# Kernel tuning notes

Measured on AMD Instinct MI355X. Metric: run time of the kernel, lower is better.

The kernel has to match this reference:

```python
import jax, jax.numpy as jnp
import numpy as np

N = 20000      # nodes
E = 320000     # edges
F = 128        # feat_dim
N_RBF = 20
CUTOFF = 5.0


def setup_inputs() -> dict:
    key = jax.random.key(0)
    ks = jax.random.split(key, 12)
    h_i = jax.random.normal(ks[0], (N, F), dtype=jnp.float32)
    v_i = jax.random.normal(ks[1], (N, F, 3), dtype=jnp.float32)
    # distances in (0, cutoff); keep strictly > 0 to avoid div-by-zero in sinc basis
    d_ij = (jax.random.uniform(ks[2], (E,), dtype=jnp.float32) * 0.98 + 0.01) * CUTOFF
    r = jax.random.normal(ks[3], (E, 3), dtype=jnp.float32)
    unit_r_ij = r / jnp.linalg.norm(r, axis=-1, keepdims=True)
    nbrs = jax.random.randint(ks[4], (E, 2), 0, N, dtype=jnp.int64)
    # params: layers = Dense(F->F, swish) then Dense(F->3F); dist_embed dense: n_rbf -> 3F
    s1 = 1.0 / np.sqrt(F)
    W1 = jax.random.uniform(ks[5], (F, F), jnp.float32, -s1, s1)
    b1 = jax.random.uniform(ks[6], (F,), jnp.float32, -s1, s1)
    W2 = jax.random.uniform(ks[7], (F, 3 * F), jnp.float32, -s1, s1)
    b2 = jax.random.uniform(ks[8], (3 * F,), jnp.float32, -s1, s1)
    sr = 1.0 / np.sqrt(N_RBF)
    Wr = jax.random.uniform(ks[9], (N_RBF, 3 * F), jnp.float32, -sr, sr)
    br = jax.random.uniform(ks[10], (3 * F,), jnp.float32, -sr, sr)
    return {"h_i": h_i, "v_i": v_i, "d_ij": d_ij, "unit_r_ij": unit_r_ij,
            "nbrs": nbrs, "W1": W1, "b1": b1, "W2": W2, "b2": b2, "Wr": Wr, "br": br}


def _dist_embed(d, Wr, br):
    # PaiNN sinc-like radial basis: sin(n*pi*d/cutoff)/d, n=1..N_RBF
    n = jnp.arange(1, N_RBF + 1, dtype=d.dtype)
    rbf = jnp.sin(n[None, :] * jnp.pi * d[:, None] / CUTOFF) / d[:, None]  # [E, N_RBF]
    # cosine cutoff envelope
    fcut = 0.5 * (jnp.cos(jnp.pi * d / CUTOFF) + 1.0) * (d < CUTOFF)       # [E]
    return (rbf @ Wr + br) * fcut[:, None]                                  # [E, 3F]


def reference(h_i, v_i, d_ij, unit_r_ij, nbrs, W1, b1, W2, b2, Wr, br):
    # phi = Dense(swish) -> Dense : [N, 3F]
    phi = jax.nn.silu(h_i @ W1 + b1) @ W2 + b2
    src = nbrs[:, 1]
    dst = nbrs[:, 0]
    edge_inv = phi[src] * _dist_embed(d_ij, Wr, br)          # [E, 3F]
    edge_inv = edge_inv.reshape(edge_inv.shape[0], 3, F)     # [E, 3, F]
    f1, f2, f3 = edge_inv[:, 0], edge_inv[:, 1], edge_inv[:, 2]
    # dv: [E, F, 3]
    dv = f1[:, :, None] * unit_r_ij[:, None, :] + f2[:, :, None] * v_i[src]
    dh_i = jax.ops.segment_sum(f3, dst, num_segments=N)      # [N, F]
    dv_i = jax.ops.segment_sum(dv, dst, num_segments=N)      # [N, F, 3]
    return (dh_i, dv_i)
```

## Files before the change

kernel.cpp:

```cpp
#include <hip/hip_runtime.h>
#include <math.h>

#define F 128
#define THREEF 384
#define N_RBF 20
#define CUTOFF 5.0f
#define CAP 64
#define TLDS_STRIDE 136

typedef __bf16 bf16x8 __attribute__((ext_vector_type(8)));
typedef float  f32x4  __attribute__((ext_vector_type(4)));

__global__ __launch_bounds__(256) void prep_kernel(
    const float* __restrict__ d_ij, const float* __restrict__ unit_r,
    const int* __restrict__ nbrs,
    const float* __restrict__ W1, const float* __restrict__ W2,
    const float* __restrict__ Wr,
    int* __restrict__ cnt, float* __restrict__ pack,
    __bf16* __restrict__ W1T, __bf16* __restrict__ W2T,
    float* __restrict__ WrT, int E, int EB)
{
    const int tid = threadIdx.x;
    const int b   = blockIdx.x;

    if (b < EB) {
        const int e = b * 256 + tid;
        if (e >= E) return;
        const int2 nb = ((const int2*)nbrs)[e];
        const int dst = nb.x;
        const int src = nb.y;
        const int slot = atomicAdd(&cnt[dst], 1);
        if (slot >= CAP) return;

        const float d = d_ij[e];
        const float x = (float)M_PI * d * (1.0f / CUTOFF);
        float sx, cx;
        __sincosf(x, &sx, &cx);
        const float fcut = (d < CUTOFF) ? 0.5f * (cx + 1.0f) : 0.0f;
        float4 q0, q1;
        q0.x = sx * fcut / d;
        q0.y = 2.0f * cx;
        q0.z = fcut;
        q0.w = unit_r[3 * e + 0];
        q1.x = unit_r[3 * e + 1];
        q1.y = unit_r[3 * e + 2];
        q1.z = __int_as_float(src);
        q1.w = 0.0f;
        float4* pk = (float4*)(pack + ((size_t)dst * CAP + slot) * 8);
        pk[0] = q0;
        pk[1] = q1;
    } else if (b < EB + 256) {
        const int idx = (b - EB) * 256 + tid;
        if (idx < 128 * 128) {
            const int n = idx >> 7, k = idx & 127;
            W1T[idx] = (__bf16)W1[k * F + n];
        }
        if (idx < 384 * 128) {
            const int n = idx >> 7, k = idx & 127;
            W2T[idx] = (__bf16)W2[k * THREEF + n];
        }
    } else {
        const int idx = (b - EB - 256) * 256 + tid;
        if (idx >= 5 * 3 * 128) return;
        const int f  = idx & 127;
        const int c  = (idx >> 7) % 3;
        const int n4 = idx / (3 * 128);
        float4 v;
        v.x = Wr[(4 * n4 + 0) * THREEF + c * 128 + f];
        v.y = Wr[(4 * n4 + 1) * THREEF + c * 128 + f];
        v.z = Wr[(4 * n4 + 2) * THREEF + c * 128 + f];
        v.w = Wr[(4 * n4 + 3) * THREEF + c * 128 + f];
        ((float4*)WrT)[idx] = v;
    }
}

__global__ __launch_bounds__(256) void mlp_mfma_kernel(
    const float* __restrict__ h,
    const __bf16* __restrict__ W1T,
    const float* __restrict__ b1,
    const __bf16* __restrict__ W2T,
    const float* __restrict__ b2,
    float* __restrict__ phi, int N)
{
    __shared__ __bf16 t_lds[4][16 * TLDS_STRIDE];

    const int wave = threadIdx.x >> 6;
    const int lane = threadIdx.x & 63;
    const int m    = lane & 15;
    const int quad = lane >> 4;
    const int node0 = blockIdx.x * 64 + wave * 16;
    if (node0 >= N) return;

    bf16x8 a1[4];
    #pragma unroll
    for (int kb = 0; kb < 4; ++kb) {
        const float* hp = h + (size_t)(node0 + m) * F + kb * 32 + quad * 8;
        const float4 x0 = *(const float4*)hp;
        const float4 x1 = *(const float4*)(hp + 4);
        bf16x8 a;
        a[0] = (__bf16)x0.x; a[1] = (__bf16)x0.y;
        a[2] = (__bf16)x0.z; a[3] = (__bf16)x0.w;
        a[4] = (__bf16)x1.x; a[5] = (__bf16)x1.y;
        a[6] = (__bf16)x1.z; a[7] = (__bf16)x1.w;
        a1[kb] = a;
    }

    #pragma unroll
    for (int ct = 0; ct < 8; ++ct) {
        f32x4 acc = {0.0f, 0.0f, 0.0f, 0.0f};
        #pragma unroll
        for (int kb = 0; kb < 4; ++kb) {
            const bf16x8 b =
                *(const bf16x8*)(W1T + (size_t)(ct * 16 + m) * F + kb * 32 + quad * 8);
            acc = __builtin_amdgcn_mfma_f32_16x16x32_bf16(a1[kb], b, acc, 0, 0, 0);
        }
        const int col = ct * 16 + m;
        const float bb = b1[col];
        #pragma unroll
        for (int reg = 0; reg < 4; ++reg) {
            const float x = acc[reg] + bb;
            const float s = x / (1.0f + __expf(-x));
            t_lds[wave][(quad * 4 + reg) * TLDS_STRIDE + col] = (__bf16)s;
        }
    }

    bf16x8 a2[4];
    #pragma unroll
    for (int kb = 0; kb < 4; ++kb)
        a2[kb] = *(const bf16x8*)&t_lds[wave][m * TLDS_STRIDE + kb * 32 + quad * 8];

    #pragma unroll
    for (int ct = 0; ct < 24; ++ct) {
        f32x4 acc = {0.0f, 0.0f, 0.0f, 0.0f};
        #pragma unroll
        for (int kb = 0; kb < 4; ++kb) {
            const bf16x8 b =
                *(const bf16x8*)(W2T + (size_t)(ct * 16 + m) * F + kb * 32 + quad * 8);
            acc = __builtin_amdgcn_mfma_f32_16x16x32_bf16(a2[kb], b, acc, 0, 0, 0);
        }
        const int col   = ct * 16 + m;
        const int plane = col >> 7;
        const int fc    = col & 127;
        const float bb  = b2[col];
        float* pp = phi + (size_t)plane * N * F + fc;
        #pragma unroll
        for (int reg = 0; reg < 4; ++reg) {
            const int row = quad * 4 + reg;
            pp[(size_t)(node0 + row) * F] = acc[reg] + bb;
        }
    }
}

__global__ __launch_bounds__(256) void gather_kernel(
    const float* __restrict__ phi,
    const float* __restrict__ v_i,
    const float* __restrict__ WrT,
    const float* __restrict__ br,
    const int*   __restrict__ cnt,
    const float* __restrict__ pack,
    float* __restrict__ dh,
    float* __restrict__ dv,
    int N)
{
    __shared__ float4 s_pack[2][CAP * 2];

    const int tid  = threadIdx.x;
    const int half = tid >> 7;
    const int f    = tid & 127;
    const int node = blockIdx.x * 2 + half;

    const int deg0 = cnt[node];
    const int deg  = deg0 < CAP ? deg0 : CAP;

    {
        const float4* src = (const float4*)(pack + (size_t)node * CAP * 8);
        if (f < 2 * deg) s_pack[half][f] = src[f];
    }
    __syncthreads();

    const float br0 = br[f], br1 = br[f + 128], br2 = br[f + 256];

    const float* phi0 = phi;
    const float* phi1 = phi + (size_t)N * F;
    const float* phi2 = phi + (size_t)2 * N * F;
    const float4* wT  = (const float4*)WrT;

    float dh_acc = 0.0f, dv0 = 0.0f, dv1 = 0.0f, dv2 = 0.0f;

    for (int i = 0; i < deg; ++i) {
        const float* q = (const float*)&s_pack[half][2 * i];
        const float s1   = q[0];
        const float twoc = q[1];
        const float fcut = q[2];
        const float ux   = q[3];
        const float uy   = q[4];
        const float uz   = q[5];
        const int src = __builtin_amdgcn_readfirstlane(__float_as_int(q[6]));

        float a0 = br0 * fcut, a1 = br1 * fcut, a2 = br2 * fcut;
        float rp = 0.0f, rc = s1;
        #pragma unroll
        for (int n4 = 0; n4 < 5; ++n4) {
            const float4 w0 = wT[(n4 * 3 + 0) * 128 + f];
            const float4 w1 = wT[(n4 * 3 + 1) * 128 + f];
            const float4 w2 = wT[(n4 * 3 + 2) * 128 + f];
            #pragma unroll
            for (int k = 0; k < 4; ++k) {
                const float wa = ((const float*)&w0)[k];
                const float wb = ((const float*)&w1)[k];
                const float wc = ((const float*)&w2)[k];
                a0 = fmaf(rc, wa, a0);
                a1 = fmaf(rc, wb, a1);
                a2 = fmaf(rc, wc, a2);
                const float rn = fmaf(twoc, rc, -rp);
                rp = rc;
                rc = rn;
            }
        }

        const float f1 = phi0[(size_t)src * F + f] * a0;
        const float f2 = phi1[(size_t)src * F + f] * a1;
        const float f3 = phi2[(size_t)src * F + f] * a2;

        dh_acc += f3;

        const float* vs = v_i + (size_t)src * THREEF + 3 * f;
        dv0 = fmaf(f1, ux, fmaf(f2, vs[0], dv0));
        dv1 = fmaf(f1, uy, fmaf(f2, vs[1], dv1));
        dv2 = fmaf(f1, uz, fmaf(f2, vs[2], dv2));
    }

    dh[(size_t)node * F + f] = dh_acc;
    float* dvp = dv + (size_t)node * THREEF + 3 * f;
    dvp[0] = dv0;
    dvp[1] = dv1;
    dvp[2] = dv2;
}

extern "C" void kernel_launch(void* const* d_in, const int* in_sizes, int n_in,
                              void* d_out, int out_size, void* d_ws, size_t ws_size,
                              hipStream_t stream) {
    const float* h_i    = (const float*)d_in[0];
    const float* v_i    = (const float*)d_in[1];
    const float* d_ij   = (const float*)d_in[2];
    const float* unit_r = (const float*)d_in[3];
    const int*   nbrs   = (const int*)  d_in[4];
    const float* W1     = (const float*)d_in[5];
    const float* b1     = (const float*)d_in[6];
    const float* W2     = (const float*)d_in[7];
    const float* b2     = (const float*)d_in[8];
    const float* Wr     = (const float*)d_in[9];
    const float* br     = (const float*)d_in[10];

    const int N = in_sizes[0] / F;
    const int E = in_sizes[2];

    float* dh = (float*)d_out;
    float* dv = dh + (size_t)N * F;

    float*  phi  = (float*)d_ws;
    float*  pack = phi + (size_t)3 * N * F;
    float*  WrT  = pack + (size_t)N * CAP * 8;
    int*    cnt  = (int*)(WrT + 5 * 3 * 128 * 4);
    __bf16* W1T  = (__bf16*)(cnt + N);
    __bf16* W2T  = W1T + 128 * 128;

    const int EB = (E + 255) / 256;

    hipMemsetAsync(cnt, 0, (size_t)N * sizeof(int), stream);

    prep_kernel<<<EB + 256 + 8, 256, 0, stream>>>(
        d_ij, unit_r, nbrs, W1, W2, Wr, cnt, pack, W1T, W2T, WrT, E, EB);
    mlp_mfma_kernel<<<(N + 63) / 64, 256, 0, stream>>>(h_i, W1T, b1, W2T, b2,
                                                       phi, N);
    gather_kernel<<<N / 2, 256, 0, stream>>>(phi, v_i, WrT, br, cnt, pack,
                                             dh, dv, N);
}
```

Baseline: 294.9 us.

## Split gather work across three thread groups per node and stage MLP stores via LDS

The gather kernel now uses one 384-thread block per node. Each 128-thread group handles one of the three phi planes (f1, f2, f3), keeps its radial weights in registers, and combines dv partials through shared memory. This spreads the per-edge RBF FMA chain and the gather loads over three times as many threads, cutting per-thread serial latency, at the cost of one block per node and a barrier. Separately, the MLP kernel stages each output plane tile in LDS and writes it out as coalesced float4 rows instead of strided scalar stores.

```diff
diff --git a/kernel.cpp b/kernel.cpp
--- a/kernel.cpp
+++ b/kernel.cpp
@@ -7,6 +7,7 @@
 #define CUTOFF 5.0f
 #define CAP 64
 #define TLDS_STRIDE 136
+#define CLDS_STRIDE 132
 
 typedef __bf16 bf16x8 __attribute__((ext_vector_type(8)));
 typedef float  f32x4  __attribute__((ext_vector_type(4)));
@@ -83,6 +84,7 @@
     float* __restrict__ phi, int N)
 {
     __shared__ __bf16 t_lds[4][16 * TLDS_STRIDE];
+    __shared__ float  c_lds[4][16 * CLDS_STRIDE];
 
     const int wave = threadIdx.x >> 6;
     const int lane = threadIdx.x & 63;
@@ -130,28 +132,36 @@
         a2[kb] = *(const bf16x8*)&t_lds[wave][m * TLDS_STRIDE + kb * 32 + quad * 8];
 
     #pragma unroll
-    for (int ct = 0; ct < 24; ++ct) {
-        f32x4 acc = {0.0f, 0.0f, 0.0f, 0.0f};
-        #pragma unroll
-        for (int kb = 0; kb < 4; ++kb) {
-            const bf16x8 b =
-                *(const bf16x8*)(W2T + (size_t)(ct * 16 + m) * F + kb * 32 + quad * 8);
-            acc = __builtin_amdgcn_mfma_f32_16x16x32_bf16(a2[kb], b, acc, 0, 0, 0);
-        }
-        const int col   = ct * 16 + m;
-        const int plane = col >> 7;
-        const int fc    = col & 127;
-        const float bb  = b2[col];
-        float* pp = phi + (size_t)plane * N * F + fc;
-        #pragma unroll
-        for (int reg = 0; reg < 4; ++reg) {
-            const int row = quad * 4 + reg;
-            pp[(size_t)(node0 + row) * F] = acc[reg] + bb;
-        }
-    }
-}
-
-__global__ __launch_bounds__(256) void gather_kernel(
+    for (int p = 0; p < 3; ++p) {
+        #pragma unroll
+        for (int ct = 0; ct < 8; ++ct) {
+            f32x4 acc = {0.0f, 0.0f, 0.0f, 0.0f};
+            #pragma unroll
+            for (int kb = 0; kb < 4; ++kb) {
+                const bf16x8 b = *(const bf16x8*)(
+                    W2T + (size_t)(p * 128 + ct * 16 + m) * F + kb * 32 + quad * 8);
+                acc = __builtin_amdgcn_mfma_f32_16x16x32_bf16(a2[kb], b, acc, 0, 0, 0);
+            }
+            const int colf = ct * 16 + m;
+            const float bb = b2[p * 128 + colf];
+            #pragma unroll
+            for (int reg = 0; reg < 4; ++reg)
+                c_lds[wave][(quad * 4 + reg) * CLDS_STRIDE + colf] = acc[reg] + bb;
+        }
+        float* pp = phi + (size_t)p * N * F;
+        #pragma unroll
+        for (int u = 0; u < 8; ++u) {
+            const int flat = u * 64 + lane;
+            const int row  = flat >> 5;
+            const int c4   = flat & 31;
+            const float4 val =
+                *(const float4*)&c_lds[wave][row * CLDS_STRIDE + c4 * 4];
+            *(float4*)&pp[(size_t)(node0 + row) * F + c4 * 4] = val;
+        }
+    }
+}
+
+__global__ __launch_bounds__(384) void gather_kernel(
     const float* __restrict__ phi,
     const float* __restrict__ v_i,
     const float* __restrict__ WrT,
@@ -162,79 +172,83 @@
     float* __restrict__ dv,
     int N)
 {
-    __shared__ float4 s_pack[2][CAP * 2];
+    __shared__ float4 s_pack[CAP * 2];
+    __shared__ float  s_dv[3][128];
 
     const int tid  = threadIdx.x;
-    const int half = tid >> 7;
+    const int g    = tid >> 7;
     const int f    = tid & 127;
-    const int node = blockIdx.x * 2 + half;
+    const int node = blockIdx.x;
 
     const int deg0 = cnt[node];
     const int deg  = deg0 < CAP ? deg0 : CAP;
 
-    {
-        const float4* src = (const float4*)(pack + (size_t)node * CAP * 8);
-        if (f < 2 * deg) s_pack[half][f] = src[f];
-    }
+    if (tid < 2 * deg)
+        s_pack[tid] = ((const float4*)(pack + (size_t)node * CAP * 8))[tid];
     __syncthreads();
 
-    const float br0 = br[f], br1 = br[f + 128], br2 = br[f + 256];
-
-    const float* phi0 = phi;
-    const float* phi1 = phi + (size_t)N * F;
-    const float* phi2 = phi + (size_t)2 * N * F;
-    const float4* wT  = (const float4*)WrT;
-
-    float dh_acc = 0.0f, dv0 = 0.0f, dv1 = 0.0f, dv2 = 0.0f;
+    const float brg = br[g * 128 + f];
+
+    float4 w[5];
+    #pragma unroll
+    for (int n4 = 0; n4 < 5; ++n4)
+        w[n4] = ((const float4*)WrT)[(n4 * 3 + g) * 128 + f];
+
+    const float* phig = phi + (size_t)g * N * F;
+
+    float acc0 = 0.0f, acc1 = 0.0f, acc2 = 0.0f;
 
     for (int i = 0; i < deg; ++i) {
-        const float* q = (const float*)&s_pack[half][2 * i];
+        const float* q = (const float*)&s_pack[2 * i];
         const float s1   = q[0];
         const float twoc = q[1];
         const float fcut = q[2];
-        const float ux   = q[3];
-        const float uy   = q[4];
-        const float uz   = q[5];
         const int src = __builtin_amdgcn_readfirstlane(__float_as_int(q[6]));
 
-        float a0 = br0 * fcut, a1 = br1 * fcut, a2 = br2 * fcut;
+        float a = brg * fcut;
         float rp = 0.0f, rc = s1;
         #pragma unroll
         for (int n4 = 0; n4 < 5; ++n4) {
-            const float4 w0 = wT[(n4 * 3 + 0) * 128 + f];
-            const float4 w1 = wT[(n4 * 3 + 1) * 128 + f];
-            const float4 w2 = wT[(n4 * 3 + 2) * 128 + f];
             #pragma unroll
             for (int k = 0; k < 4; ++k) {
-                const float wa = ((const float*)&w0)[k];
-                const float wb = ((const float*)&w1)[k];
-                const float wc = ((const float*)&w2)[k];
-                a0 = fmaf(rc, wa, a0);
-                a1 = fmaf(rc, wb, a1);
-                a2 = fmaf(rc, wc, a2);
+                a = fmaf(rc, ((const float*)&w[n4])[k], a);
                 const float rn = fmaf(twoc, rc, -rp);
                 rp = rc;
                 rc = rn;
             }
         }
 
-        const float f1 = phi0[(size_t)src * F + f] * a0;
-        const float f2 = phi1[(size_t)src * F + f] * a1;
-        const float f3 = phi2[(size_t)src * F + f] * a2;
-
-        dh_acc += f3;
-
-        const float* vs = v_i + (size_t)src * THREEF + 3 * f;
-        dv0 = fmaf(f1, ux, fmaf(f2, vs[0], dv0));
-        dv1 = fmaf(f1, uy, fmaf(f2, vs[1], dv1));
-        dv2 = fmaf(f1, uz, fmaf(f2, vs[2], dv2));
-    }
-
-    dh[(size_t)node * F + f] = dh_acc;
-    float* dvp = dv + (size_t)node * THREEF + 3 * f;
-    dvp[0] = dv0;
-    dvp[1] = dv1;
-    dvp[2] = dv2;
+        const float fg = phig[(size_t)src * F + f] * a;
+
+        if (g == 0) {
+            acc0 = fmaf(fg, q[3], acc0);
+            acc1 = fmaf(fg, q[4], acc1);
+            acc2 = fmaf(fg, q[5], acc2);
+        } else if (g == 1) {
+            const float* vs = v_i + (size_t)src * THREEF + 3 * f;
+            acc0 = fmaf(fg, vs[0], acc0);
+            acc1 = fmaf(fg, vs[1], acc1);
+            acc2 = fmaf(fg, vs[2], acc2);
+        } else {
+            acc0 += fg;
+        }
+    }
+
+    if (g == 0) {
+        s_dv[0][f] = acc0;
+        s_dv[1][f] = acc1;
+        s_dv[2][f] = acc2;
+    }
+    __syncthreads();
+
+    if (g == 1) {
+        float* dvp = dv + (size_t)node * THREEF + 3 * f;
+        dvp[0] = s_dv[0][f] + acc0;
+        dvp[1] = s_dv[1][f] + acc1;
+        dvp[2] = s_dv[2][f] + acc2;
+    } else if (g == 2) {
+        dh[(size_t)node * F + f] = acc0;
+    }
 }
 
 extern "C" void kernel_launch(void* const* d_in, const int* in_sizes, int n_in,
@@ -273,6 +287,6 @@
         d_ij, unit_r, nbrs, W1, W2, Wr, cnt, pack, W1T, W2T, WrT, E, EB);
     mlp_mfma_kernel<<<(N + 63) / 64, 256, 0, stream>>>(h_i, W1T, b1, W2T, b2,
                                                        phi, N);
-    gather_kernel<<<N / 2, 256, 0, stream>>>(phi, v_i, WrT, br, cnt, pack,
-                                             dh, dv, N);
-}
+    gather_kernel<<<N, 384, 0, stream>>>(phi, v_i, WrT, br, cnt, pack,
+                                         dh, dv, N);
+}
```

Measured after the change: 402.9 us. 36.6% more time.
